# Optimization experiments

Measured on AMD Instinct MI355X. Metric: run time of the kernel, lower is better.

## Reference

```python
import jax, jax.numpy as jnp
import numpy as np

N_GENE = 100000
N_DIS = 20000
H = 128
E = 500000


def setup_inputs() -> dict:
    key = jax.random.key(0)
    ks = jax.random.split(key, 12)
    s1 = 1.0 / np.sqrt(2 * H)  # fan-in init scale, Linear(2H, H)
    s2 = 1.0 / np.sqrt(H)      # fan-in init scale, Linear(H, 1)
    z_gene = jax.random.normal(ks[0], (N_GENE, H), jnp.float32)
    z_disease = jax.random.normal(ks[1], (N_DIS, H), jnp.float32)
    # gene->disease edges: row indexes genes, col indexes diseases
    edges_gd = jnp.stack([
        jax.random.randint(ks[2], (E,), 0, N_GENE),
        jax.random.randint(ks[3], (E,), 0, N_DIS),
    ])
    # gene->gene edges
    edges_gg = jnp.stack([
        jax.random.randint(ks[4], (E,), 0, N_GENE),
        jax.random.randint(ks[5], (E,), 0, N_GENE),
    ])
    return {
        "z_gene": z_gene,
        "z_disease": z_disease,
        "edges_gd": edges_gd,
        "edges_gg": edges_gg,
        "w1_gd": jax.random.normal(ks[6], (2 * H, H), jnp.float32) * s1,
        "b1_gd": jnp.zeros((H,), jnp.float32),
        "w2_gd": jax.random.normal(ks[7], (H, 1), jnp.float32) * s2,
        "b2_gd": jnp.zeros((1,), jnp.float32),
        "w1_gg": jax.random.normal(ks[8], (2 * H, H), jnp.float32) * s1,
        "b1_gg": jnp.zeros((H,), jnp.float32),
        "w2_gg": jax.random.normal(ks[9], (H, 1), jnp.float32) * s2,
        "b2_gg": jnp.zeros((1,), jnp.float32),
    }


def _decode(z_src, z_dst, edges, w1, b1, w2, b2):
    # gather src/dst node embeddings by edge index, concat -> [E, 2H]
    z = jnp.concatenate([z_src[edges[0]], z_dst[edges[1]]], axis=1)
    h = jnp.maximum(z @ w1 + b1, 0.0)  # Linear + ReLU
    return h @ w2 + b2                  # Linear -> [E, 1]


def reference(z_gene, z_disease, edges_gd, edges_gg,
              w1_gd, b1_gd, w2_gd, b2_gd,
              w1_gg, b1_gg, w2_gg, b2_gg):
    out_gd = _decode(z_gene, z_disease, edges_gd, w1_gd, b1_gd, w2_gd, b2_gd)
    out_gg = _decode(z_gene, z_gene, edges_gg, w1_gg, b1_gg, w2_gg, b2_gg)
    # dict of per-relation outputs in the original; stack since E matches
    return jnp.stack([out_gd, out_gg])  # [2, E, 1]
```

## Files before the change

### kernel.cpp

```cpp
#include <hip/hip_runtime.h>
#include <hip/hip_bf16.h>

#define HDIM 128

typedef __attribute__((ext_vector_type(8))) short short8;
typedef __attribute__((ext_vector_type(4))) float floatx4;

__device__ __forceinline__ float bf2f(unsigned short u) {
    return __uint_as_float(((unsigned)u) << 16);
}
__device__ __forceinline__ unsigned short f2b(float f) {
    __hip_bfloat16 h = __float2bfloat16(f);
    return __builtin_bit_cast(unsigned short, h);
}
__device__ __forceinline__ float ldv(const void* p, size_t i, int flag) {
    return flag ? bf2f(((const unsigned short*)p)[i]) : ((const float*)p)[i];
}
__device__ __forceinline__ short8 pack8(float4 a, float4 b) {
    short8 r;
    r[0] = (short)f2b(a.x); r[1] = (short)f2b(a.y);
    r[2] = (short)f2b(a.z); r[3] = (short)f2b(a.w);
    r[4] = (short)f2b(b.x); r[5] = (short)f2b(b.y);
    r[6] = (short)f2b(b.z); r[7] = (short)f2b(b.w);
    return r;
}

__device__ __forceinline__ int local_detect(const unsigned short* zbits) {
    __shared__ int red[256];
    int tid = threadIdx.x;
    int cnt = 0;
    for (int i = tid; i < 4096; i += 256) {
        int ex = (zbits[i] >> 7) & 0xFF;
        if (ex >= 100 && ex <= 140) cnt++;
    }
    red[tid] = cnt;
    __syncthreads();
    for (int s = 128; s > 0; s >>= 1) {
        if (tid < s) red[tid] += red[tid + s];
        __syncthreads();
    }
    return (red[0] >= 3686) ? 1 : 0;
}

__global__ __launch_bounds__(256) void prep_kernel(
    const unsigned short* __restrict__ zbits,
    const void* __restrict__ w1_gd, const void* __restrict__ w1_gg,
    const void* __restrict__ b1_gd, const void* __restrict__ w2_gd,
    const void* __restrict__ b2_gd, const void* __restrict__ b1_gg,
    const void* __restrict__ w2_gg, const void* __restrict__ b2_gg,
    unsigned short* __restrict__ img, float* __restrict__ params,
    int* __restrict__ flagout)
{
    int flag = local_detect(zbits);
    int b = blockIdx.x;
    if (b < 4) {
        const void* w1 = (b < 2) ? w1_gd : w1_gg;
        int part = b & 1;
        unsigned short* out = img + b * 16384;
        for (int idx = threadIdx.x; idx < 16384; idx += 256) {
            int n   = idx >> 7;
            int rem = idx & 127;
            int g   = (rem >> 3) ^ (n & 15);
            int j   = rem & 7;
            size_t s = (size_t)(part * 128 + g * 8 + j) * 128 + n;
            out[idx] = flag ? ((const unsigned short*)w1)[s]
                            : f2b(((const float*)w1)[s]);
        }
    } else {
        int t = threadIdx.x;
        if (t < 128) {
            params[t]       = ldv(b1_gd, t, flag);
            params[256 + t] = ldv(b1_gg, t, flag);
        } else {
            params[t]       = ldv(w2_gd, t - 128, flag);
            params[256 + t] = ldv(w2_gg, t - 128, flag);
        }
        if (t == 0) {
            params[512] = ldv(b2_gd, 0, flag);
            params[513] = ldv(b2_gg, 0, flag);
            *flagout = flag;
        }
    }
}

__global__ __launch_bounds__(256) void proj_all_kernel(
    const void* __restrict__ Zg, const void* __restrict__ Zd,
    const uint4* __restrict__ Wimg, const float* __restrict__ params,
    unsigned short* __restrict__ A_gd, unsigned short* __restrict__ B_gd,
    unsigned short* __restrict__ A_gg, unsigned short* __restrict__ B_gg,
    int NG, int ND, int gblk, const int* __restrict__ flagp)
{
    __shared__ uint4 sW[2048];
    int tid  = threadIdx.x;
    int lane = tid & 63;
    int wave = tid >> 6;
    int nl   = lane & 15;
    int quad = lane >> 4;
    int flag = *flagp;

    bool gene = (int)blockIdx.x < gblk;
    int blk = gene ? blockIdx.x : blockIdx.x - gblk;
    int M = gene ? NG : ND;
    const void* Z = gene ? Zg : Zd;

    int row = blk * 64 + wave * 16 + nl;
    int rc = row < M ? row : (M - 1);

    short8 zf[4];
    if (flag) {
        const uint4* z = (const uint4*)Z + (size_t)rc * 16;
#pragma unroll
        for (int kc = 0; kc < 4; ++kc)
            zf[kc] = __builtin_bit_cast(short8, z[kc * 4 + quad]);
    } else {
        const float4* z = (const float4*)Z + (size_t)rc * 32;
#pragma unroll
        for (int kc = 0; kc < 4; ++kc) {
            int o = kc * 8 + quad * 2;
            zf[kc] = pack8(z[o], z[o + 1]);
        }
    }

    int nph = gene ? 3 : 1;
    for (int ph = 0; ph < nph; ++ph) {
        const uint4* im;
        unsigned short* Out;
        const float* bias;
        if (gene) {
            im   = Wimg + (ph == 0 ? 0 : ph == 1 ? 2 : 3) * 2048;
            Out  = ph == 0 ? A_gd : ph == 1 ? A_gg : B_gg;
            bias = ph == 0 ? params : ph == 1 ? params + 256 : nullptr;
        } else {
            im = Wimg + 2048; Out = B_gd; bias = nullptr;
        }
        __syncthreads();
#pragma unroll
        for (int i = 0; i < 8; ++i) sW[tid + i * 256] = im[tid + i * 256];
        __syncthreads();

        floatx4 acc[8];
#pragma unroll
        for (int nt = 0; nt < 8; ++nt) acc[nt] = (floatx4){0.f, 0.f, 0.f, 0.f};
#pragma unroll
        for (int kc = 0; kc < 4; ++kc) {
            int p = (kc * 4 + quad) ^ nl;
#pragma unroll
            for (int nt = 0; nt < 8; ++nt) {
                short8 wf = __builtin_bit_cast(short8, sW[(nt * 16 + nl) * 16 + p]);
                acc[nt] = __builtin_amdgcn_mfma_f32_16x16x32_bf16(wf, zf[kc], acc[nt], 0, 0, 0);
            }
        }
        if (row < M) {
#pragma unroll
            for (int nt = 0; nt < 8; ++nt) {
                float4 bv = {0.f, 0.f, 0.f, 0.f};
                if (bias) bv = *(const float4*)(bias + nt * 16 + quad * 4);
                ushort4 v;
                v.x = f2b(acc[nt][0] + bv.x);
                v.y = f2b(acc[nt][1] + bv.y);
                v.z = f2b(acc[nt][2] + bv.z);
                v.w = f2b(acc[nt][3] + bv.w);
                *(ushort4*)(Out + (size_t)row * HDIM + nt * 16 + quad * 4) = v;
            }
        }
    }
}

__global__ __launch_bounds__(256) void edge_kernel(
    const int* __restrict__ edges_gd, const int* __restrict__ edges_gg,
    const unsigned short* __restrict__ A_gd, const unsigned short* __restrict__ B_gd,
    const unsigned short* __restrict__ A_gg, const unsigned short* __restrict__ B_gg,
    const float* __restrict__ params,
    void* __restrict__ out, int E, int nb, const int* __restrict__ flagp)
{
    int rel = ((int)blockIdx.x >= nb) ? 1 : 0;
    int e = (blockIdx.x - rel * nb) * 256 + threadIdx.x;
    if (e >= E) return;

    const int* edges = rel ? edges_gg : edges_gd;
    const unsigned short* A = rel ? A_gg : A_gd;
    const unsigned short* B = rel ? B_gg : B_gd;
    const float* w2 = params + 128 + rel * 256;
    float b2 = params[512 + rel];

    int src = edges[e];
    int dst = edges[E + e];
    const uint4* ar = (const uint4*)(A + (size_t)src * HDIM);
    const uint4* br = (const uint4*)(B + (size_t)dst * HDIM);

    float acc = 0.f;
#pragma unroll
    for (int g = 0; g < 4; ++g) {
        uint4 a[4], b[4];
#pragma unroll
        for (int i = 0; i < 4; ++i) { a[i] = ar[g * 4 + i]; b[i] = br[g * 4 + i]; }
#pragma unroll
        for (int i = 0; i < 4; ++i) {
            const unsigned* au = (const unsigned*)&a[i];
            const unsigned* bu = (const unsigned*)&b[i];
#pragma unroll
            for (int j = 0; j < 4; ++j) {
                int ch = g * 32 + i * 8 + j * 2;
                float x0 = __uint_as_float(au[j] << 16);
                float x1 = __uint_as_float(au[j] & 0xffff0000u);
                float y0 = __uint_as_float(bu[j] << 16);
                float y1 = __uint_as_float(bu[j] & 0xffff0000u);
                float h0 = fmaxf(x0 + y0, 0.f);
                float h1 = fmaxf(x1 + y1, 0.f);
                acc = fmaf(h0, w2[ch], acc);
                acc = fmaf(h1, w2[ch + 1], acc);
            }
        }
    }
    float r = acc + b2;
    size_t o = (size_t)rel * E + e;
    if (*flagp) ((unsigned short*)out)[o] = f2b(r);
    else        ((float*)out)[o] = r;
}

__global__ __launch_bounds__(256) void detect_kernel(
    const unsigned short* __restrict__ zbits, int* __restrict__ flag)
{
    int f = local_detect(zbits);
    if (threadIdx.x == 0) *flag = f;
}

__global__ __launch_bounds__(128) void naive_edge_kernel(
    const int* __restrict__ edges,
    const void* __restrict__ zsrc, const void* __restrict__ zdst,
    const void* __restrict__ w1, const void* __restrict__ b1,
    const void* __restrict__ w2, const void* __restrict__ b2,
    void* __restrict__ out, size_t eoff, int E,
    const int* __restrict__ flagp)
{
    int flag = flagp ? *flagp : 0;
    __shared__ float zs[128], zd[128], red[128];
    int e = blockIdx.x;
    int n = threadIdx.x;
    int src = edges[e], dst = edges[E + e];
    zs[n] = ldv(zsrc, (size_t)src * HDIM + n, flag);
    zd[n] = ldv(zdst, (size_t)dst * HDIM + n, flag);
    __syncthreads();
    float acc = ldv(b1, n, flag);
    for (int k = 0; k < 128; ++k) acc = fmaf(zs[k], ldv(w1, (size_t)k * HDIM + n, flag), acc);
    for (int k = 0; k < 128; ++k) acc = fmaf(zd[k], ldv(w1, (size_t)(128 + k) * HDIM + n, flag), acc);
    red[n] = fmaxf(acc, 0.f) * ldv(w2, n, flag);
    __syncthreads();
    for (int s = 64; s > 0; s >>= 1) {
        if (n < s) red[n] += red[n + s];
        __syncthreads();
    }
    if (n == 0) {
        float r = red[0] + ldv(b2, 0, flag);
        if (flag) ((unsigned short*)out)[eoff + e] = f2b(r);
        else      ((float*)out)[eoff + e] = r;
    }
}

extern "C" void kernel_launch(void* const* d_in, const int* in_sizes, int n_in,
                              void* d_out, int out_size, void* d_ws, size_t ws_size,
                              hipStream_t stream)
{
    const void* z_gene = d_in[0];
    const void* z_dis  = d_in[1];
    const int* edges_gd = (const int*)d_in[2];
    const int* edges_gg = (const int*)d_in[3];
    const void* w1_gd = d_in[4];
    const void* b1_gd = d_in[5];
    const void* w2_gd = d_in[6];
    const void* b2_gd = d_in[7];
    const void* w1_gg = d_in[8];
    const void* b1_gg = d_in[9];
    const void* w2_gg = d_in[10];
    const void* b2_gg = d_in[11];

    int NG = in_sizes[0] / HDIM;
    int ND = in_sizes[1] / HDIM;
    int E  = in_sizes[2] / 2;

    size_t off_flag   = 0;
    size_t off_params = 256;
    size_t off_img    = 2560;
    size_t off_Agd    = off_img + 131072;
    size_t off_Bgd    = off_Agd + (size_t)NG * HDIM * 2;
    size_t off_Agg    = off_Bgd + (size_t)ND * HDIM * 2;
    size_t off_Bgg    = off_Agg + (size_t)NG * HDIM * 2;
    size_t need       = off_Bgg + (size_t)NG * HDIM * 2;

    char* ws = (char*)d_ws;

    if (ws_size < need) {
        const int* flagp = nullptr;
        if (ws_size >= 16) {
            detect_kernel<<<1, 256, 0, stream>>>((const unsigned short*)z_gene, (int*)ws);
            flagp = (const int*)ws;
        }
        naive_edge_kernel<<<E, 128, 0, stream>>>(edges_gd, z_gene, z_dis,
                                                 w1_gd, b1_gd, w2_gd, b2_gd,
                                                 d_out, 0, E, flagp);
        naive_edge_kernel<<<E, 128, 0, stream>>>(edges_gg, z_gene, z_gene,
                                                 w1_gg, b1_gg, w2_gg, b2_gg,
                                                 d_out, (size_t)E, E, flagp);
        return;
    }

    int* flag = (int*)(ws + off_flag);
    float* params = (float*)(ws + off_params);
    unsigned short* img = (unsigned short*)(ws + off_img);
    unsigned short* Agd = (unsigned short*)(ws + off_Agd);
    unsigned short* Bgd = (unsigned short*)(ws + off_Bgd);
    unsigned short* Agg = (unsigned short*)(ws + off_Agg);
    unsigned short* Bgg = (unsigned short*)(ws + off_Bgg);

    prep_kernel<<<5, 256, 0, stream>>>((const unsigned short*)z_gene,
                                       w1_gd, w1_gg, b1_gd, w2_gd, b2_gd,
                                       b1_gg, w2_gg, b2_gg, img, params, flag);

    const uint4* img4 = (const uint4*)img;
    int gblk = (NG + 63) / 64;
    int dblk = (ND + 63) / 64;
    proj_all_kernel<<<gblk + dblk, 256, 0, stream>>>(z_gene, z_dis, img4, params,
                                                     Agd, Bgd, Agg, Bgg,
                                                     NG, ND, gblk, flag);

    int nb = (E + 255) / 256;
    edge_kernel<<<2 * nb, 256, 0, stream>>>(edges_gd, edges_gg, Agd, Bgd, Agg, Bgg,
                                            params, d_out, E, nb, flag);
}
```

Measured before the change: 262.1 us.

## Parallelize weight prep, double rows per projection wave, cooperative edge gather

The weight-image prep kernel is split across 32 blocks instead of 4, each handling a slice of k, so the transpose-and-swizzle finishes sooner. The projection kernel has each wave process two 16-row tiles, reusing each shared-memory weight fragment for two MFMAs and halving the number of blocks that reload the weight image. The edge kernel changes from one thread per edge (128-channel serial loads) to 8 lanes per edge pair, each lane loading 32 contiguous bytes of both rows, with a shuffle reduction. This gives coalesced gathers and more memory-level parallelism, at the cost of extra shuffles and higher register use.

```diff
diff --git a/kernel.cpp b/kernel.cpp
--- a/kernel.cpp
+++ b/kernel.cpp
@@ -53,29 +53,31 @@
 {
     int flag = local_detect(zbits);
     int b = blockIdx.x;
-    if (b < 4) {
-        const void* w1 = (b < 2) ? w1_gd : w1_gg;
-        int part = b & 1;
-        unsigned short* out = img + b * 16384;
-        for (int idx = threadIdx.x; idx < 16384; idx += 256) {
-            int n   = idx >> 7;
-            int rem = idx & 127;
-            int g   = (rem >> 3) ^ (n & 15);
-            int j   = rem & 7;
-            size_t s = (size_t)(part * 128 + g * 8 + j) * 128 + n;
-            out[idx] = flag ? ((const unsigned short*)w1)[s]
-                            : f2b(((const float*)w1)[s]);
+    int tid = threadIdx.x;
+    if (b < 32) {
+        int im   = b >> 3;
+        int sub  = b & 7;
+        const void* w1 = (im < 2) ? w1_gd : w1_gg;
+        int part = im & 1;
+        unsigned short* out = img + im * 16384;
+        int n = tid & 127;
+#pragma unroll
+        for (int it = 0; it < 8; ++it) {
+            int k = sub * 16 + it * 2 + (tid >> 7);
+            unsigned short v = flag
+                ? ((const unsigned short*)w1)[(size_t)(part * 128 + k) * 128 + n]
+                : f2b(((const float*)w1)[(size_t)(part * 128 + k) * 128 + n]);
+            out[n * 128 + (((k >> 3) ^ (n & 15)) << 3) + (k & 7)] = v;
         }
     } else {
-        int t = threadIdx.x;
-        if (t < 128) {
-            params[t]       = ldv(b1_gd, t, flag);
-            params[256 + t] = ldv(b1_gg, t, flag);
+        if (tid < 128) {
+            params[tid]       = ldv(b1_gd, tid, flag);
+            params[256 + tid] = ldv(b1_gg, tid, flag);
         } else {
-            params[t]       = ldv(w2_gd, t - 128, flag);
-            params[256 + t] = ldv(w2_gg, t - 128, flag);
-        }
-        if (t == 0) {
+            params[tid]       = ldv(w2_gd, tid - 128, flag);
+            params[256 + tid] = ldv(w2_gg, tid - 128, flag);
+        }
+        if (tid == 0) {
             params[512] = ldv(b2_gd, 0, flag);
             params[513] = ldv(b2_gg, 0, flag);
             *flagout = flag;
@@ -103,21 +105,28 @@
     int M = gene ? NG : ND;
     const void* Z = gene ? Zg : Zd;
 
-    int row = blk * 64 + wave * 16 + nl;
-    int rc = row < M ? row : (M - 1);
-
-    short8 zf[4];
+    int row0 = blk * 128 + wave * 32 + nl;
+    int row1 = row0 + 16;
+    int r0c = row0 < M ? row0 : (M - 1);
+    int r1c = row1 < M ? row1 : (M - 1);
+
+    short8 zf[2][4];
     if (flag) {
-        const uint4* z = (const uint4*)Z + (size_t)rc * 16;
-#pragma unroll
-        for (int kc = 0; kc < 4; ++kc)
-            zf[kc] = __builtin_bit_cast(short8, z[kc * 4 + quad]);
+        const uint4* z0 = (const uint4*)Z + (size_t)r0c * 16;
+        const uint4* z1 = (const uint4*)Z + (size_t)r1c * 16;
+#pragma unroll
+        for (int kc = 0; kc < 4; ++kc) {
+            zf[0][kc] = __builtin_bit_cast(short8, z0[kc * 4 + quad]);
+            zf[1][kc] = __builtin_bit_cast(short8, z1[kc * 4 + quad]);
+        }
     } else {
-        const float4* z = (const float4*)Z + (size_t)rc * 32;
+        const float4* z0 = (const float4*)Z + (size_t)r0c * 32;
+        const float4* z1 = (const float4*)Z + (size_t)r1c * 32;
 #pragma unroll
         for (int kc = 0; kc < 4; ++kc) {
             int o = kc * 8 + quad * 2;
-            zf[kc] = pack8(z[o], z[o + 1]);
+            zf[0][kc] = pack8(z0[o], z0[o + 1]);
+            zf[1][kc] = pack8(z1[o], z1[o + 1]);
         }
     }
 
@@ -138,29 +147,38 @@
         for (int i = 0; i < 8; ++i) sW[tid + i * 256] = im[tid + i * 256];
         __syncthreads();
 
-        floatx4 acc[8];
-#pragma unroll
-        for (int nt = 0; nt < 8; ++nt) acc[nt] = (floatx4){0.f, 0.f, 0.f, 0.f};
+        floatx4 acc[2][8];
+#pragma unroll
+        for (int rt = 0; rt < 2; ++rt)
+#pragma unroll
+            for (int nt = 0; nt < 8; ++nt)
+                acc[rt][nt] = (floatx4){0.f, 0.f, 0.f, 0.f};
+
 #pragma unroll
         for (int kc = 0; kc < 4; ++kc) {
             int p = (kc * 4 + quad) ^ nl;
 #pragma unroll
             for (int nt = 0; nt < 8; ++nt) {
                 short8 wf = __builtin_bit_cast(short8, sW[(nt * 16 + nl) * 16 + p]);
-                acc[nt] = __builtin_amdgcn_mfma_f32_16x16x32_bf16(wf, zf[kc], acc[nt], 0, 0, 0);
+                acc[0][nt] = __builtin_amdgcn_mfma_f32_16x16x32_bf16(wf, zf[0][kc], acc[0][nt], 0, 0, 0);
+                acc[1][nt] = __builtin_amdgcn_mfma_f32_16x16x32_bf16(wf, zf[1][kc], acc[1][nt], 0, 0, 0);
             }
         }
-        if (row < M) {
-#pragma unroll
-            for (int nt = 0; nt < 8; ++nt) {
-                float4 bv = {0.f, 0.f, 0.f, 0.f};
-                if (bias) bv = *(const float4*)(bias + nt * 16 + quad * 4);
-                ushort4 v;
-                v.x = f2b(acc[nt][0] + bv.x);
-                v.y = f2b(acc[nt][1] + bv.y);
-                v.z = f2b(acc[nt][2] + bv.z);
-                v.w = f2b(acc[nt][3] + bv.w);
-                *(ushort4*)(Out + (size_t)row * HDIM + nt * 16 + quad * 4) = v;
+#pragma unroll
+        for (int rt = 0; rt < 2; ++rt) {
+            int row = rt ? row1 : row0;
+            if (row < M) {
+#pragma unroll
+                for (int nt = 0; nt < 8; ++nt) {
+                    float4 bv = {0.f, 0.f, 0.f, 0.f};
+                    if (bias) bv = *(const float4*)(bias + nt * 16 + quad * 4);
+                    ushort4 v;
+                    v.x = f2b(acc[rt][nt][0] + bv.x);
+                    v.y = f2b(acc[rt][nt][1] + bv.y);
+                    v.z = f2b(acc[rt][nt][2] + bv.z);
+                    v.w = f2b(acc[rt][nt][3] + bv.w);
+                    *(ushort4*)(Out + (size_t)row * HDIM + nt * 16 + quad * 4) = v;
+                }
             }
         }
     }
@@ -174,48 +192,90 @@
     void* __restrict__ out, int E, int nb, const int* __restrict__ flagp)
 {
     int rel = ((int)blockIdx.x >= nb) ? 1 : 0;
-    int e = (blockIdx.x - rel * nb) * 256 + threadIdx.x;
-    if (e >= E) return;
-
+    int blk = blockIdx.x - rel * nb;
     const int* edges = rel ? edges_gg : edges_gd;
     const unsigned short* A = rel ? A_gg : A_gd;
     const unsigned short* B = rel ? B_gg : B_gd;
     const float* w2 = params + 128 + rel * 256;
     float b2 = params[512 + rel];
 
-    int src = edges[e];
-    int dst = edges[E + e];
-    const uint4* ar = (const uint4*)(A + (size_t)src * HDIM);
-    const uint4* br = (const uint4*)(B + (size_t)dst * HDIM);
-
-    float acc = 0.f;
-#pragma unroll
-    for (int g = 0; g < 4; ++g) {
-        uint4 a[4], b[4];
-#pragma unroll
-        for (int i = 0; i < 4; ++i) { a[i] = ar[g * 4 + i]; b[i] = br[g * 4 + i]; }
-#pragma unroll
-        for (int i = 0; i < 4; ++i) {
-            const unsigned* au = (const unsigned*)&a[i];
-            const unsigned* bu = (const unsigned*)&b[i];
-#pragma unroll
-            for (int j = 0; j < 4; ++j) {
-                int ch = g * 32 + i * 8 + j * 2;
-                float x0 = __uint_as_float(au[j] << 16);
-                float x1 = __uint_as_float(au[j] & 0xffff0000u);
-                float y0 = __uint_as_float(bu[j] << 16);
-                float y1 = __uint_as_float(bu[j] & 0xffff0000u);
-                float h0 = fmaxf(x0 + y0, 0.f);
-                float h1 = fmaxf(x1 + y1, 0.f);
-                acc = fmaf(h0, w2[ch], acc);
-                acc = fmaf(h1, w2[ch + 1], acc);
-            }
-        }
-    }
-    float r = acc + b2;
-    size_t o = (size_t)rel * E + e;
-    if (*flagp) ((unsigned short*)out)[o] = f2b(r);
-    else        ((float*)out)[o] = r;
+    int tid  = threadIdx.x;
+    int lane = tid & 63;
+    int wave = tid >> 6;
+    int nl   = lane & 7;
+    int grp  = lane >> 3;
+
+    float w2f[16];
+#pragma unroll
+    for (int i = 0; i < 4; ++i) {
+        float4 t = *(const float4*)(w2 + nl * 16 + i * 4);
+        w2f[i * 4 + 0] = t.x; w2f[i * 4 + 1] = t.y;
+        w2f[i * 4 + 2] = t.z; w2f[i * 4 + 3] = t.w;
+    }
+
+    int e0 = blk * 64 + (wave * 8 + grp) * 2;
+    int e1 = e0 + 1;
+    int emax = E - 2 > 0 ? E - 2 : 0;
+    int ec = e0 < emax ? e0 : emax;
+    int sel = e0 - ec;
+    int2 sp = *(const int2*)(edges + ec);
+    int2 dp = *(const int2*)(edges + E + ec);
+    int src0 = sel ? sp.y : sp.x;
+    int dst0 = sel ? dp.y : dp.x;
+    int src1 = sp.y;
+    int dst1 = dp.y;
+
+    const uint4* a0p = (const uint4*)(A + (size_t)src0 * HDIM) + nl * 2;
+    const uint4* b0p = (const uint4*)(B + (size_t)dst0 * HDIM) + nl * 2;
+    const uint4* a1p = (const uint4*)(A + (size_t)src1 * HDIM) + nl * 2;
+    const uint4* b1p = (const uint4*)(B + (size_t)dst1 * HDIM) + nl * 2;
+    uint4 a0[2] = {a0p[0], a0p[1]};
+    uint4 c0[2] = {b0p[0], b0p[1]};
+    uint4 a1[2] = {a1p[0], a1p[1]};
+    uint4 c1[2] = {b1p[0], b1p[1]};
+
+    float acc0 = 0.f, acc1 = 0.f;
+#pragma unroll
+    for (int i = 0; i < 2; ++i) {
+        const unsigned* au0 = (const unsigned*)&a0[i];
+        const unsigned* cu0 = (const unsigned*)&c0[i];
+        const unsigned* au1 = (const unsigned*)&a1[i];
+        const unsigned* cu1 = (const unsigned*)&c1[i];
+#pragma unroll
+        for (int j = 0; j < 4; ++j) {
+            int ch = i * 8 + j * 2;
+            float x0 = __uint_as_float(au0[j] << 16);
+            float x1 = __uint_as_float(au0[j] & 0xffff0000u);
+            float y0 = __uint_as_float(cu0[j] << 16);
+            float y1 = __uint_as_float(cu0[j] & 0xffff0000u);
+            acc0 = fmaf(fmaxf(x0 + y0, 0.f), w2f[ch], acc0);
+            acc0 = fmaf(fmaxf(x1 + y1, 0.f), w2f[ch + 1], acc0);
+            float u0 = __uint_as_float(au1[j] << 16);
+            float u1 = __uint_as_float(au1[j] & 0xffff0000u);
+            float v0 = __uint_as_float(cu1[j] << 16);
+            float v1 = __uint_as_float(cu1[j] & 0xffff0000u);
+            acc1 = fmaf(fmaxf(u0 + v0, 0.f), w2f[ch], acc1);
+            acc1 = fmaf(fmaxf(u1 + v1, 0.f), w2f[ch + 1], acc1);
+        }
+    }
+    acc0 += __shfl_xor(acc0, 1); acc1 += __shfl_xor(acc1, 1);
+    acc0 += __shfl_xor(acc0, 2); acc1 += __shfl_xor(acc1, 2);
+    acc0 += __shfl_xor(acc0, 4); acc1 += __shfl_xor(acc1, 4);
+
+    if (nl == 0) {
+        int flag = *flagp;
+        size_t base = (size_t)rel * E;
+        if (e0 < E) {
+            float r = acc0 + b2;
+            if (flag) ((unsigned short*)out)[base + e0] = f2b(r);
+            else      ((float*)out)[base + e0] = r;
+        }
+        if (e1 < E) {
+            float r = acc1 + b2;
+            if (flag) ((unsigned short*)out)[base + e1] = f2b(r);
+            else      ((float*)out)[base + e1] = r;
+        }
+    }
 }
 
 __global__ __launch_bounds__(256) void detect_kernel(
@@ -312,18 +372,18 @@
     unsigned short* Agg = (unsigned short*)(ws + off_Agg);
     unsigned short* Bgg = (unsigned short*)(ws + off_Bgg);
 
-    prep_kernel<<<5, 256, 0, stream>>>((const unsigned short*)z_gene,
-                                       w1_gd, w1_gg, b1_gd, w2_gd, b2_gd,
-                                       b1_gg, w2_gg, b2_gg, img, params, flag);
+    prep_kernel<<<33, 256, 0, stream>>>((const unsigned short*)z_gene,
+                                        w1_gd, w1_gg, b1_gd, w2_gd, b2_gd,
+                                        b1_gg, w2_gg, b2_gg, img, params, flag);
 
     const uint4* img4 = (const uint4*)img;
-    int gblk = (NG + 63) / 64;
-    int dblk = (ND + 63) / 64;
+    int gblk = (NG + 127) / 128;
+    int dblk = (ND + 127) / 128;
     proj_all_kernel<<<gblk + dblk, 256, 0, stream>>>(z_gene, z_dis, img4, params,
                                                      Agd, Bgd, Agg, Bgg,
                                                      NG, ND, gblk, flag);
 
-    int nb = (E + 255) / 256;
+    int nb = (E + 63) / 64;
     edge_kernel<<<2 * nb, 256, 0, stream>>>(edges_gd, edges_gg, Agd, Bgd, Agg, Bgg,
                                             params, d_out, E, nb, flag);
 }
```

New measurement: 226.6 us. -13.6%, faster.
